# Performance work log

Hardware: AMD Instinct MI355X
Metric: run time of the kernel (lower is better)

The kernel has to match this reference:

```python
import jax, jax.numpy as jnp
import numpy as np

N = 100000      # num_nodes
E = 3200000     # num_edges (avg degree 32)
DIN, DH, DOUT = 128, 128, 64
S, L = 3, 3     # num_scales, num_layers
EPS = 1e-5


def setup_inputs() -> dict:
    key = jax.random.key(0)
    ks = jax.random.split(key, 12)
    sc = 0.05
    x = jax.random.normal(ks[0], (N, DIN), jnp.float32)
    edge_index = jax.random.randint(ks[1], (2, E), 0, N, jnp.int32)
    return {
        'x': x,
        'edge_index': edge_index,
        'W0': jax.random.normal(ks[2], (S, DIN, DH), jnp.float32) * sc,
        'b0': jnp.zeros((S, DH), jnp.float32),
        'W1': jax.random.normal(ks[3], (S, DH, DH), jnp.float32) * sc,
        'b1': jnp.zeros((S, DH), jnp.float32),
        'W2': jax.random.normal(ks[4], (S, DH, DOUT), jnp.float32) * sc,
        'b2': jnp.zeros((S, DOUT), jnp.float32),
        'gamma': jnp.ones((S * L, DH), jnp.float32),   # layer_norms (only first L-1 per scale used)
        'beta': jnp.zeros((S * L, DH), jnp.float32),
        'Wf': jax.random.normal(ks[5], (S * DOUT, DOUT), jnp.float32) * sc,
        'bf': jnp.zeros((DOUT,), jnp.float32),
    }


def _layer_norm(h, g, b):
    mu = jnp.mean(h, axis=-1, keepdims=True)
    var = jnp.mean(jnp.square(h - mu), axis=-1, keepdims=True)
    return (h - mu) * jax.lax.rsqrt(var + EPS) * g + b


def _gcn(h, W, b, src, dst, dis):
    # GCNConv: D^{-1/2}(A+I)D^{-1/2} h W + b  (self-loops handled separately)
    hw = h @ W
    msg = hw[src] * (dis[src] * dis[dst])[:, None]          # gather + edge-scale
    agg = jax.ops.segment_sum(msg, dst, num_segments=N)     # scatter-add
    agg = agg + hw * (dis * dis)[:, None]                   # self-loop term
    return agg + b


def reference(x, edge_index, W0, b0, W1, b1, W2, b2, gamma, beta, Wf, bf):
    src, dst = edge_index[0], edge_index[1]
    # degree on A + I (unit edge weights + self loop)
    deg = jax.ops.segment_sum(jnp.ones((E,), x.dtype), dst, num_segments=N) + 1.0
    dis = jax.lax.rsqrt(deg)

    scale_outputs = []
    for s in range(S):
        h = _gcn(x, W0[s], b0[s], src, dst, dis)
        h = _layer_norm(jax.nn.relu(h), gamma[s * L + 0], beta[s * L + 0])  # dropout=identity (eval)
        h = _gcn(h, W1[s], b1[s], src, dst, dis)
        h = _layer_norm(jax.nn.relu(h), gamma[s * L + 1], beta[s * L + 1])
        h = _gcn(h, W2[s], b2[s], src, dst, dis)
        scale_outputs.append(h)

    fused = jnp.concatenate(scale_outputs, axis=-1)  # [N, S*DOUT]
    return fused @ Wf + bf
```

## Files before the change

### kernel.cpp

```cpp
#include <hip/hip_runtime.h>

#define DIN 128
#define DH 128
#define DOUTC 64
#define NS 3
#define NL 3
#define EPSV 1e-5f

typedef __attribute__((ext_vector_type(8))) short bf16x8;
typedef __attribute__((ext_vector_type(4))) float f32x4;

static __device__ inline float bf2f(unsigned short h) {
    unsigned int u = ((unsigned int)h) << 16;
    return __builtin_bit_cast(float, u);
}
static __device__ inline unsigned short f2bf(float f) {
    unsigned int u = __builtin_bit_cast(unsigned int, f);
    u += 0x7fffu + ((u >> 16) & 1u);
    return (unsigned short)(u >> 16);
}
static __device__ inline float lo16(unsigned int u) {
    return __builtin_bit_cast(float, u << 16);
}
static __device__ inline float hi16(unsigned int u) {
    return __builtin_bit_cast(float, u & 0xffff0000u);
}

__global__ __launch_bounds__(256) void k_count_r(const int* __restrict__ dst,
                                                 int* __restrict__ counts, int e, int n) {
    int rg = blockIdx.x & 7;
    int lo = rg * (n >> 3);
    int hi = (rg == 7) ? n : lo + (n >> 3);
    int nb = gridDim.x >> 3, bi = blockIdx.x >> 3;
    int e4 = e >> 2;
    const int4* dst4 = (const int4*)dst;
    for (int i = bi * 256 + threadIdx.x; i < e4; i += nb * 256) {
        int4 d = dst4[i];
        if (d.x >= lo && d.x < hi) atomicAdd(&counts[d.x], 1);
        if (d.y >= lo && d.y < hi) atomicAdd(&counts[d.y], 1);
        if (d.z >= lo && d.z < hi) atomicAdd(&counts[d.z], 1);
        if (d.w >= lo && d.w < hi) atomicAdd(&counts[d.w], 1);
    }
    if (bi == 0 && (int)threadIdx.x < (e & 3)) {
        int d = dst[e4 * 4 + threadIdx.x];
        if (d >= lo && d < hi) atomicAdd(&counts[d], 1);
    }
}

__global__ void k_dis(const int* __restrict__ counts, float* __restrict__ dis, int n) {
    int i = blockIdx.x * blockDim.x + threadIdx.x;
    if (i < n) dis[i] = rsqrtf((float)counts[i] + 1.0f);
}

__global__ void k_scanA(const int* __restrict__ counts, int* __restrict__ row_start,
                        int* __restrict__ bsums, int n) {
    __shared__ int s[512];
    int t = threadIdx.x;
    int i = blockIdx.x * 512 + t;
    int v = (i < n) ? counts[i] : 0;
    s[t] = v;
    __syncthreads();
    for (int off = 1; off < 512; off <<= 1) {
        int x = s[t];
        if (t >= off) x += s[t - off];
        __syncthreads();
        s[t] = x;
        __syncthreads();
    }
    if (i < n) row_start[i] = s[t] - v;
    if (t == 511) bsums[blockIdx.x] = s[511];
}

__global__ void k_scanB(int* __restrict__ bsums, int nb) {
    __shared__ int s[256];
    int t = threadIdx.x;
    int v = (t < nb) ? bsums[t] : 0;
    s[t] = v;
    __syncthreads();
    for (int off = 1; off < 256; off <<= 1) {
        int x = s[t];
        if (t >= off) x += s[t - off];
        __syncthreads();
        s[t] = x;
        __syncthreads();
    }
    if (t < nb) bsums[t] = s[t] - v;
}

__global__ void k_scanC(int* __restrict__ row_start, const int* __restrict__ bsums, int n) {
    int i = blockIdx.x * blockDim.x + threadIdx.x;
    if (i < n) row_start[i] += bsums[i >> 9];
}

__global__ __launch_bounds__(256) void k_fill_r(const int* __restrict__ src,
                                                const int* __restrict__ dst,
                                                int* __restrict__ cursor,
                                                int* __restrict__ col, int e, int n) {
    int rg = blockIdx.x & 7;
    int lo = rg * (n >> 3);
    int hi = (rg == 7) ? n : lo + (n >> 3);
    int nb = gridDim.x >> 3, bi = blockIdx.x >> 3;
    int e4 = e >> 2;
    const int4* dst4 = (const int4*)dst;
    const int4* src4 = (const int4*)src;
    for (int i = bi * 256 + threadIdx.x; i < e4; i += nb * 256) {
        int4 d = dst4[i];
        int4 s = src4[i];
        if (d.x >= lo && d.x < hi) col[atomicAdd(&cursor[d.x], 1)] = s.x;
        if (d.y >= lo && d.y < hi) col[atomicAdd(&cursor[d.y], 1)] = s.y;
        if (d.z >= lo && d.z < hi) col[atomicAdd(&cursor[d.z], 1)] = s.z;
        if (d.w >= lo && d.w < hi) col[atomicAdd(&cursor[d.w], 1)] = s.w;
    }
    if (bi == 0 && (int)threadIdx.x < (e & 3)) {
        int d = dst[e4 * 4 + threadIdx.x];
        int s = src[e4 * 4 + threadIdx.x];
        if (d >= lo && d < hi) col[atomicAdd(&cursor[d], 1)] = s;
    }
}

__global__ void k_prep_w(const float* __restrict__ W0, const float* __restrict__ W1,
                         const float* __restrict__ W2, const float* __restrict__ Wf,
                         const float* __restrict__ b2, const float* __restrict__ bf,
                         unsigned short* __restrict__ Wt0hi, unsigned short* __restrict__ Wt0lo,
                         unsigned short* __restrict__ Wt1hi, unsigned short* __restrict__ Wt1lo,
                         unsigned short* __restrict__ Mhi, unsigned short* __restrict__ Mlo,
                         float* __restrict__ bcomb) {
    int idx = blockIdx.x * blockDim.x + threadIdx.x;
    if (idx < NS * DH * DH) {
        int s = idx / (DH * DH);
        int rem = idx % (DH * DH);
        int o = rem / DH, i = rem % DH;
        {
            float v = W0[(size_t)s * DH * DH + (size_t)i * DH + o];
            unsigned short h = f2bf(v);
            Wt0hi[idx] = h;
            Wt0lo[idx] = f2bf(v - bf2f(h));
        }
        {
            float v = W1[(size_t)s * DH * DH + (size_t)i * DH + o];
            unsigned short h = f2bf(v);
            Wt1hi[idx] = h;
            Wt1lo[idx] = f2bf(v - bf2f(h));
        }
    }
    if (idx < DOUTC * NS * DH) {
        int o = idx / (NS * DH);
        int k = idx % (NS * DH);
        int s = k / DH, i = k % DH;
        float acc = 0.f;
        for (int c = 0; c < DOUTC; ++c)
            acc += W2[((size_t)s * DH + i) * DOUTC + c] * Wf[((size_t)s * DOUTC + c) * DOUTC + o];
        unsigned short h = f2bf(acc);
        Mhi[idx] = h;
        Mlo[idx] = f2bf(acc - bf2f(h));
    }
    if (idx < DOUTC) {
        float acc = bf[idx];
        for (int s = 0; s < NS; ++s)
            for (int c = 0; c < DOUTC; ++c)
                acc += b2[s * DOUTC + c] * Wf[((size_t)s * DOUTC + c) * DOUTC + idx];
        bcomb[idx] = acc;
    }
}

__global__ void k_cvt(const float2* __restrict__ x, unsigned int* __restrict__ xb,
                      const float* __restrict__ dis, int m) {
    int i = blockIdx.x * blockDim.x + threadIdx.x;
    int stride = gridDim.x * blockDim.x;
    for (; i < m; i += stride) {
        float d = dis[i >> 6];
        float2 v = x[i];
        xb[i] = ((unsigned int)f2bf(v.y * d) << 16) | f2bf(v.x * d);
    }
}

__global__ __launch_bounds__(256) void k_agg128(
        const unsigned int* __restrict__ in, unsigned int* __restrict__ out,
        const float* __restrict__ dis, const int* __restrict__ rowstart,
        const int* __restrict__ counts, const int* __restrict__ col, int n) {
    int wid = (blockIdx.x * blockDim.x + threadIdx.x) >> 6;
    int lane = threadIdx.x & 63;
    int nw = (gridDim.x * blockDim.x) >> 6;
    for (int v = wid; v < n; v += nw) {
        float dv = dis[v];
        const int* colp = col + rowstart[v];
        int cnt = counts[v];
        unsigned int us = in[(size_t)v * 64 + lane];
        float a0 = lo16(us), a1 = hi16(us);
        int i = 0;
        for (; i + 4 <= cnt; i += 4) {
            int s0 = colp[i], s1 = colp[i + 1], s2 = colp[i + 2], s3 = colp[i + 3];
            unsigned int u0 = in[(size_t)s0 * 64 + lane];
            unsigned int u1 = in[(size_t)s1 * 64 + lane];
            unsigned int u2 = in[(size_t)s2 * 64 + lane];
            unsigned int u3 = in[(size_t)s3 * 64 + lane];
            a0 += lo16(u0); a1 += hi16(u0);
            a0 += lo16(u1); a1 += hi16(u1);
            a0 += lo16(u2); a1 += hi16(u2);
            a0 += lo16(u3); a1 += hi16(u3);
        }
        for (; i < cnt; ++i) {
            unsigned int u0 = in[(size_t)colp[i] * 64 + lane];
            a0 += lo16(u0); a1 += hi16(u0);
        }
        out[(size_t)v * 64 + lane] = ((unsigned int)f2bf(dv * a1) << 16) | f2bf(dv * a0);
    }
}

__global__ __launch_bounds__(256) void k_agg384(
        const unsigned int* __restrict__ in, unsigned int* __restrict__ out,
        const float* __restrict__ dis, const int* __restrict__ rowstart,
        const int* __restrict__ counts, const int* __restrict__ col, int n) {
    int wid = (blockIdx.x * blockDim.x + threadIdx.x) >> 6;
    int lane = threadIdx.x & 63;
    int nw = (gridDim.x * blockDim.x) >> 6;
    for (int v = wid; v < n; v += nw) {
        float dv = dis[v];
        const int* colp = col + rowstart[v];
        int cnt = counts[v];
        const unsigned int* ps = in + (size_t)v * 192;
        unsigned int us0 = ps[lane], us1 = ps[lane + 64], us2 = ps[lane + 128];
        float a0 = lo16(us0), a1 = hi16(us0);
        float a2 = lo16(us1), a3 = hi16(us1);
        float a4 = lo16(us2), a5 = hi16(us2);
        int i = 0;
        for (; i + 4 <= cnt; i += 4) {
            int s0 = colp[i], s1 = colp[i + 1], s2 = colp[i + 2], s3 = colp[i + 3];
            const unsigned int* p0 = in + (size_t)s0 * 192;
            const unsigned int* p1 = in + (size_t)s1 * 192;
            const unsigned int* p2 = in + (size_t)s2 * 192;
            const unsigned int* p3 = in + (size_t)s3 * 192;
            unsigned int u00 = p0[lane], u01 = p0[lane + 64], u02 = p0[lane + 128];
            unsigned int u10 = p1[lane], u11 = p1[lane + 64], u12 = p1[lane + 128];
            unsigned int u20 = p2[lane], u21 = p2[lane + 64], u22 = p2[lane + 128];
            unsigned int u30 = p3[lane], u31 = p3[lane + 64], u32 = p3[lane + 128];
            a0 += lo16(u00); a1 += hi16(u00);
            a2 += lo16(u01); a3 += hi16(u01);
            a4 += lo16(u02); a5 += hi16(u02);
            a0 += lo16(u10); a1 += hi16(u10);
            a2 += lo16(u11); a3 += hi16(u11);
            a4 += lo16(u12); a5 += hi16(u12);
            a0 += lo16(u20); a1 += hi16(u20);
            a2 += lo16(u21); a3 += hi16(u21);
            a4 += lo16(u22); a5 += hi16(u22);
            a0 += lo16(u30); a1 += hi16(u30);
            a2 += lo16(u31); a3 += hi16(u31);
            a4 += lo16(u32); a5 += hi16(u32);
        }
        for (; i < cnt; ++i) {
            const unsigned int* p0 = in + (size_t)colp[i] * 192;
            unsigned int u00 = p0[lane], u01 = p0[lane + 64], u02 = p0[lane + 128];
            a0 += lo16(u00); a1 += hi16(u00);
            a2 += lo16(u01); a3 += hi16(u01);
            a4 += lo16(u02); a5 += hi16(u02);
        }
        unsigned int* po = out + (size_t)v * 192;
        po[lane]       = ((unsigned int)f2bf(dv * a1) << 16) | f2bf(dv * a0);
        po[lane + 64]  = ((unsigned int)f2bf(dv * a3) << 16) | f2bf(dv * a2);
        po[lane + 128] = ((unsigned int)f2bf(dv * a5) << 16) | f2bf(dv * a4);
    }
}

__global__ __launch_bounds__(256) void k_agg64(
        const unsigned int* __restrict__ in, float* __restrict__ out,
        const float* __restrict__ bcomb, const float* __restrict__ dis,
        const int* __restrict__ rowstart, const int* __restrict__ counts,
        const int* __restrict__ col, int n) {
    int wid = (blockIdx.x * blockDim.x + threadIdx.x) >> 6;
    int lane = threadIdx.x & 63;
    int half = lane >> 5, c = lane & 31;
    int nw = (gridDim.x * blockDim.x) >> 6;
    float bc0 = bcomb[c * 2], bc1 = bcomb[c * 2 + 1];
    for (int w = wid; w * 2 < n; w += nw) {
        int v = w * 2 + half;
        if (v >= n) continue;
        float dv = dis[v];
        const int* colp = col + rowstart[v];
        int cnt = counts[v];
        unsigned int us = in[(size_t)v * 32 + c];
        float a0 = lo16(us), a1 = hi16(us);
        int i = 0;
        for (; i + 4 <= cnt; i += 4) {
            int s0 = colp[i], s1 = colp[i + 1], s2 = colp[i + 2], s3 = colp[i + 3];
            unsigned int u0 = in[(size_t)s0 * 32 + c];
            unsigned int u1 = in[(size_t)s1 * 32 + c];
            unsigned int u2 = in[(size_t)s2 * 32 + c];
            unsigned int u3 = in[(size_t)s3 * 32 + c];
            a0 += lo16(u0); a1 += hi16(u0);
            a0 += lo16(u1); a1 += hi16(u1);
            a0 += lo16(u2); a1 += hi16(u2);
            a0 += lo16(u3); a1 += hi16(u3);
        }
        for (; i < cnt; ++i) {
            unsigned int u0 = in[(size_t)colp[i] * 32 + c];
            a0 += lo16(u0); a1 += hi16(u0);
        }
        float2 o = make_float2(dv * a0 + bc0, dv * a1 + bc1);
        *(float2*)&out[(size_t)v * 64 + c * 2] = o;
    }
}

__global__ __launch_bounds__(256) void k_gemm0(
        const unsigned short* __restrict__ A, const unsigned short* __restrict__ Whi,
        const unsigned short* __restrict__ Wlo, const float* __restrict__ bias,
        const float* __restrict__ gamma, const float* __restrict__ beta,
        const float* __restrict__ dis, unsigned short* __restrict__ out, int n) {
    int wave = threadIdx.x >> 6, lane = threadIdx.x & 63;
    int g = blockIdx.x * 4 + wave;
    if (g * 16 >= n) return;
    int r16 = lane & 15, g4 = lane >> 4;
    int row = g * 16 + r16;
    if (row >= n) row = n - 1;

    bf16x8 a[4];
    #pragma unroll
    for (int ks = 0; ks < 4; ++ks)
        a[ks] = *(const bf16x8*)&A[(size_t)row * DH + ks * 32 + g4 * 8];

    for (int s = 0; s < NS; ++s) {
        const unsigned short* whi = Whi + (size_t)s * DH * DH;
        const unsigned short* wlo = Wlo + (size_t)s * DH * DH;
        f32x4 acc[8];
        #pragma unroll
        for (int t = 0; t < 8; ++t) acc[t] = (f32x4){0.f, 0.f, 0.f, 0.f};
        #pragma unroll
        for (int ks = 0; ks < 4; ++ks) {
            #pragma unroll
            for (int t = 0; t < 8; ++t) {
                size_t wofs = (size_t)(t * 16 + r16) * DH + ks * 32 + g4 * 8;
                bf16x8 bh = *(const bf16x8*)&whi[wofs];
                bf16x8 bl = *(const bf16x8*)&wlo[wofs];
                acc[t] = __builtin_amdgcn_mfma_f32_16x16x32_bf16(a[ks], bh, acc[t], 0, 0, 0);
                acc[t] = __builtin_amdgcn_mfma_f32_16x16x32_bf16(a[ks], bl, acc[t], 0, 0, 0);
            }
        }
        float bia[8], gam[8], bet[8];
        #pragma unroll
        for (int t = 0; t < 8; ++t) {
            bia[t] = bias[s * DH + t * 16 + r16];
            gam[t] = gamma[(size_t)(s * NL + 0) * DH + t * 16 + r16];
            bet[t] = beta[(size_t)(s * NL + 0) * DH + t * 16 + r16];
        }
        #pragma unroll
        for (int r = 0; r < 4; ++r) {
            float y[8];
            float sm = 0.f, q = 0.f;
            #pragma unroll
            for (int t = 0; t < 8; ++t) {
                y[t] = fmaxf(acc[t][r] + bia[t], 0.f);
                sm += y[t];
                q += y[t] * y[t];
            }
            #pragma unroll
            for (int off = 8; off; off >>= 1) {
                sm += __shfl_xor(sm, off);
                q += __shfl_xor(q, off);
            }
            float mu = sm * (1.f / 128.f);
            float var = q * (1.f / 128.f) - mu * mu;
            float rstd = rsqrtf(var + EPSV);
            int node = g * 16 + g4 * 4 + r;
            if (node < n) {
                float dnode = dis[node];
                #pragma unroll
                for (int t = 0; t < 8; ++t) {
                    float o = ((y[t] - mu) * rstd * gam[t] + bet[t]) * dnode;
                    out[(size_t)node * (NS * DH) + s * DH + t * 16 + r16] = f2bf(o);
                }
            }
        }
    }
}

__global__ __launch_bounds__(256) void k_gemm1q(
        const unsigned short* __restrict__ G, const unsigned short* __restrict__ Whi,
        const unsigned short* __restrict__ Wlo, const unsigned short* __restrict__ Mhi,
        const unsigned short* __restrict__ Mlo, const float* __restrict__ bias,
        const float* __restrict__ gamma, const float* __restrict__ beta,
        const float* __restrict__ dis, unsigned short* __restrict__ q, int n) {
    __shared__ __align__(16) unsigned short sH[4][16][392];
    int wave = threadIdx.x >> 6, lane = threadIdx.x & 63;
    int g = blockIdx.x * 4 + wave;
    if (g * 16 >= n) return;
    int r16 = lane & 15, g4 = lane >> 4;
    int row = g * 16 + r16;
    if (row >= n) row = n - 1;

    for (int s = 0; s < NS; ++s) {
        bf16x8 a[4];
        #pragma unroll
        for (int ks = 0; ks < 4; ++ks)
            a[ks] = *(const bf16x8*)&G[(size_t)row * (NS * DH) + s * DH + ks * 32 + g4 * 8];
        const unsigned short* whi = Whi + (size_t)s * DH * DH;
        const unsigned short* wlo = Wlo + (size_t)s * DH * DH;
        f32x4 acc[8];
        #pragma unroll
        for (int t = 0; t < 8; ++t) acc[t] = (f32x4){0.f, 0.f, 0.f, 0.f};
        #pragma unroll
        for (int ks = 0; ks < 4; ++ks) {
            #pragma unroll
            for (int t = 0; t < 8; ++t) {
                size_t wofs = (size_t)(t * 16 + r16) * DH + ks * 32 + g4 * 8;
                bf16x8 bh = *(const bf16x8*)&whi[wofs];
                bf16x8 bl = *(const bf16x8*)&wlo[wofs];
                acc[t] = __builtin_amdgcn_mfma_f32_16x16x32_bf16(a[ks], bh, acc[t], 0, 0, 0);
                acc[t] = __builtin_amdgcn_mfma_f32_16x16x32_bf16(a[ks], bl, acc[t], 0, 0, 0);
            }
        }
        float bia[8], gam[8], bet[8];
        #pragma unroll
        for (int t = 0; t < 8; ++t) {
            bia[t] = bias[s * DH + t * 16 + r16];
            gam[t] = gamma[(size_t)(s * NL + 1) * DH + t * 16 + r16];
            bet[t] = beta[(size_t)(s * NL + 1) * DH + t * 16 + r16];
        }
        #pragma unroll
        for (int r = 0; r < 4; ++r) {
            float y[8];
            float sm = 0.f, qq = 0.f;
            #pragma unroll
            for (int t = 0; t < 8; ++t) {
                y[t] = fmaxf(acc[t][r] + bia[t], 0.f);
                sm += y[t];
                qq += y[t] * y[t];
            }
            #pragma unroll
            for (int off = 8; off; off >>= 1) {
                sm += __shfl_xor(sm, off);
                qq += __shfl_xor(qq, off);
            }
            float mu = sm * (1.f / 128.f);
            float var = qq * (1.f / 128.f) - mu * mu;
            float rstd = rsqrtf(var + EPSV);
            #pragma unroll
            for (int t = 0; t < 8; ++t) {
                float o = (y[t] - mu) * rstd * gam[t] + bet[t];
                sH[wave][g4 * 4 + r][s * DH + t * 16 + r16] = f2bf(o);
            }
        }
    }
    __syncthreads();
    f32x4 qa[4];
    #pragma unroll
    for (int t = 0; t < 4; ++t) qa[t] = (f32x4){0.f, 0.f, 0.f, 0.f};
    #pragma unroll
    for (int ks = 0; ks < 12; ++ks) {
        bf16x8 av = *(const bf16x8*)&sH[wave][r16][ks * 32 + g4 * 8];
        #pragma unroll
        for (int t = 0; t < 4; ++t) {
            size_t wofs = (size_t)(t * 16 + r16) * (NS * DH) + ks * 32 + g4 * 8;
            bf16x8 bh = *(const bf16x8*)&Mhi[wofs];
            bf16x8 bl = *(const bf16x8*)&Mlo[wofs];
            qa[t] = __builtin_amdgcn_mfma_f32_16x16x32_bf16(av, bh, qa[t], 0, 0, 0);
            qa[t] = __builtin_amdgcn_mfma_f32_16x16x32_bf16(av, bl, qa[t], 0, 0, 0);
        }
    }
    #pragma unroll
    for (int r = 0; r < 4; ++r) {
        int node = g * 16 + g4 * 4 + r;
        if (node < n) {
            float dnode = dis[node];
            #pragma unroll
            for (int t = 0; t < 4; ++t)
                q[(size_t)node * DOUTC + t * 16 + r16] = f2bf(qa[t][r] * dnode);
        }
    }
}

extern "C" void kernel_launch(void* const* d_in, const int* in_sizes, int n_in,
                              void* d_out, int out_size, void* d_ws, size_t ws_size,
                              hipStream_t stream) {
    const float* x    = (const float*)d_in[0];
    const int*   ei   = (const int*)d_in[1];
    const float* W0   = (const float*)d_in[2];
    const float* b0   = (const float*)d_in[3];
    const float* W1   = (const float*)d_in[4];
    const float* b1   = (const float*)d_in[5];
    const float* W2   = (const float*)d_in[6];
    const float* b2   = (const float*)d_in[7];
    const float* gamma= (const float*)d_in[8];
    const float* beta = (const float*)d_in[9];
    const float* Wf   = (const float*)d_in[10];
    const float* bf   = (const float*)d_in[11];
    float* out = (float*)d_out;

    const int n = in_sizes[0] / DIN;
    const int e = in_sizes[1] / 2;
    const int* src = ei;
    const int* dst = ei + e;

    char* ws = (char*)d_ws;
    auto alloc = [&](size_t bytes) {
        char* p = ws;
        ws += (bytes + 255) & ~(size_t)255;
        return p;
    };
    int*   counts   = (int*)alloc((size_t)n * 4);
    int*   cursor   = (int*)alloc((size_t)n * 4);
    int*   rowstart = (int*)alloc((size_t)n * 4);
    int*   bsums    = (int*)alloc(4096);
    float* dis      = (float*)alloc((size_t)n * 4);
    int*   col      = (int*)alloc((size_t)e * 4);
    unsigned short* Wt0hi = (unsigned short*)alloc((size_t)NS * DH * DH * 2);
    unsigned short* Wt0lo = (unsigned short*)alloc((size_t)NS * DH * DH * 2);
    unsigned short* Wt1hi = (unsigned short*)alloc((size_t)NS * DH * DH * 2);
    unsigned short* Wt1lo = (unsigned short*)alloc((size_t)NS * DH * DH * 2);
    unsigned short* Mhi   = (unsigned short*)alloc((size_t)DOUTC * NS * DH * 2);
    unsigned short* Mlo   = (unsigned short*)alloc((size_t)DOUTC * NS * DH * 2);
    float* bcomb    = (float*)alloc(DOUTC * 4);
    unsigned short* xb    = (unsigned short*)alloc((size_t)n * DIN * 2);
    unsigned short* z0    = (unsigned short*)alloc((size_t)n * DH * 2);
    unsigned short* h1cat = (unsigned short*)alloc((size_t)n * NS * DH * 2);
    unsigned short* g1cat = (unsigned short*)alloc((size_t)n * NS * DH * 2);
    unsigned short* q     = (unsigned short*)alloc((size_t)n * DOUTC * 2);

    hipMemsetAsync(counts, 0, (size_t)n * 4, stream);

    k_count_r<<<2048, 256, 0, stream>>>(dst, counts, e, n);
    k_dis<<<(n + 255) / 256, 256, 0, stream>>>(counts, dis, n);

    int nb = (n + 511) / 512;
    k_scanA<<<nb, 512, 0, stream>>>(counts, rowstart, bsums, n);
    k_scanB<<<1, 256, 0, stream>>>(bsums, nb);
    k_scanC<<<(n + 255) / 256, 256, 0, stream>>>(rowstart, bsums, n);
    hipMemcpyAsync(cursor, rowstart, (size_t)n * 4, hipMemcpyDeviceToDevice, stream);
    k_fill_r<<<2048, 256, 0, stream>>>(src, dst, cursor, col, e, n);

    k_prep_w<<<(NS * DH * DH + 255) / 256, 256, 0, stream>>>(
        W0, W1, W2, Wf, b2, bf, Wt0hi, Wt0lo, Wt1hi, Wt1lo, Mhi, Mlo, bcomb);
    k_cvt<<<2048, 256, 0, stream>>>((const float2*)x, (unsigned int*)xb, dis, n * DIN / 2);

    k_agg128<<<2048, 256, 0, stream>>>((const unsigned int*)xb, (unsigned int*)z0,
                                       dis, rowstart, counts, col, n);
    const int GG = (n / 16 + 3) / 4;
    k_gemm0<<<GG, 256, 0, stream>>>(z0, Wt0hi, Wt0lo, b0, gamma, beta, dis, h1cat, n);
    k_agg384<<<2048, 256, 0, stream>>>((const unsigned int*)h1cat, (unsigned int*)g1cat,
                                       dis, rowstart, counts, col, n);
    k_gemm1q<<<GG, 256, 0, stream>>>(g1cat, Wt1hi, Wt1lo, Mhi, Mlo,
                                     b1, gamma, beta, dis, q, n);
    k_agg64<<<2048, 256, 0, stream>>>((const unsigned int*)q, out, bcomb,
                                      dis, rowstart, counts, col, n);
}
```

Measured before the change: 1.403 ms.

## Quantize gathered node features to int8 with per-row scales in all aggregations

New measurement: 1.242 ms. 1.13x faster.

```diff
diff --git a/kernel.cpp b/kernel.cpp
--- a/kernel.cpp
+++ b/kernel.cpp
@@ -24,6 +24,17 @@
 }
 static __device__ inline float hi16(unsigned int u) {
     return __builtin_bit_cast(float, u & 0xffff0000u);
+}
+static __device__ inline unsigned int pkbf(float lo, float hi) {
+    return ((unsigned int)f2bf(hi) << 16) | f2bf(lo);
+}
+static __device__ inline float sext8(unsigned int u, int k) {
+    return (float)((int)(u << (24 - 8 * k)) >> 24);
+}
+static __device__ inline unsigned int pk8(float a, float b, float c, float d, float qs) {
+    int q0 = (int)rintf(a * qs), q1 = (int)rintf(b * qs);
+    int q2 = (int)rintf(c * qs), q3 = (int)rintf(d * qs);
+    return (q0 & 255) | ((q1 & 255) << 8) | ((q2 & 255) << 16) | ((q3 & 255) << 24);
 }
 
 __global__ __launch_bounds__(256) void k_count_r(const int* __restrict__ dst,
@@ -163,140 +174,223 @@
     }
 }
 
-__global__ void k_cvt(const float2* __restrict__ x, unsigned int* __restrict__ xb,
-                      const float* __restrict__ dis, int m) {
-    int i = blockIdx.x * blockDim.x + threadIdx.x;
-    int stride = gridDim.x * blockDim.x;
-    for (; i < m; i += stride) {
-        float d = dis[i >> 6];
-        float2 v = x[i];
-        xb[i] = ((unsigned int)f2bf(v.y * d) << 16) | f2bf(v.x * d);
-    }
-}
-
-__global__ __launch_bounds__(256) void k_agg128(
-        const unsigned int* __restrict__ in, unsigned int* __restrict__ out,
-        const float* __restrict__ dis, const int* __restrict__ rowstart,
-        const int* __restrict__ counts, const int* __restrict__ col, int n) {
-    int wid = (blockIdx.x * blockDim.x + threadIdx.x) >> 6;
+__global__ __launch_bounds__(256) void k_cvtq(const float2* __restrict__ x,
+                                              unsigned int* __restrict__ xq,
+                                              float* __restrict__ xs,
+                                              const float* __restrict__ dis, int n) {
+    int wid = ((blockIdx.x * blockDim.x + threadIdx.x) >> 6);
     int lane = threadIdx.x & 63;
-    int nw = (gridDim.x * blockDim.x) >> 6;
-    for (int v = wid; v < n; v += nw) {
-        float dv = dis[v];
-        const int* colp = col + rowstart[v];
-        int cnt = counts[v];
-        unsigned int us = in[(size_t)v * 64 + lane];
-        float a0 = lo16(us), a1 = hi16(us);
-        int i = 0;
-        for (; i + 4 <= cnt; i += 4) {
-            int s0 = colp[i], s1 = colp[i + 1], s2 = colp[i + 2], s3 = colp[i + 3];
-            unsigned int u0 = in[(size_t)s0 * 64 + lane];
-            unsigned int u1 = in[(size_t)s1 * 64 + lane];
-            unsigned int u2 = in[(size_t)s2 * 64 + lane];
-            unsigned int u3 = in[(size_t)s3 * 64 + lane];
-            a0 += lo16(u0); a1 += hi16(u0);
-            a0 += lo16(u1); a1 += hi16(u1);
-            a0 += lo16(u2); a1 += hi16(u2);
-            a0 += lo16(u3); a1 += hi16(u3);
-        }
-        for (; i < cnt; ++i) {
-            unsigned int u0 = in[(size_t)colp[i] * 64 + lane];
-            a0 += lo16(u0); a1 += hi16(u0);
-        }
-        out[(size_t)v * 64 + lane] = ((unsigned int)f2bf(dv * a1) << 16) | f2bf(dv * a0);
-    }
-}
-
-__global__ __launch_bounds__(256) void k_agg384(
-        const unsigned int* __restrict__ in, unsigned int* __restrict__ out,
-        const float* __restrict__ dis, const int* __restrict__ rowstart,
-        const int* __restrict__ counts, const int* __restrict__ col, int n) {
-    int wid = (blockIdx.x * blockDim.x + threadIdx.x) >> 6;
+    if (wid >= n) return;
+    float2 v = x[(size_t)wid * 64 + lane];
+    float m = fmaxf(fabsf(v.x), fabsf(v.y));
+    #pragma unroll
+    for (int off = 32; off; off >>= 1) m = fmaxf(m, __shfl_xor(m, off));
+    float qs = m > 0.f ? 127.f / m : 0.f;
+    int q0 = (int)rintf(v.x * qs), q1 = (int)rintf(v.y * qs);
+    ((unsigned short*)xq)[(size_t)wid * 64 + lane] =
+        (unsigned short)((q0 & 255) | ((q1 & 255) << 8));
+    if (lane == 0) xs[wid] = dis[wid] * m * (1.f / 127.f);
+}
+
+__global__ __launch_bounds__(256) void k_quant384(const unsigned int* __restrict__ h,
+                                                  unsigned int* __restrict__ hq,
+                                                  float* __restrict__ hs, int n) {
+    int wid = ((blockIdx.x * blockDim.x + threadIdx.x) >> 6);
     int lane = threadIdx.x & 63;
-    int nw = (gridDim.x * blockDim.x) >> 6;
-    for (int v = wid; v < n; v += nw) {
-        float dv = dis[v];
-        const int* colp = col + rowstart[v];
-        int cnt = counts[v];
-        const unsigned int* ps = in + (size_t)v * 192;
-        unsigned int us0 = ps[lane], us1 = ps[lane + 64], us2 = ps[lane + 128];
-        float a0 = lo16(us0), a1 = hi16(us0);
-        float a2 = lo16(us1), a3 = hi16(us1);
-        float a4 = lo16(us2), a5 = hi16(us2);
-        int i = 0;
-        for (; i + 4 <= cnt; i += 4) {
-            int s0 = colp[i], s1 = colp[i + 1], s2 = colp[i + 2], s3 = colp[i + 3];
-            const unsigned int* p0 = in + (size_t)s0 * 192;
-            const unsigned int* p1 = in + (size_t)s1 * 192;
-            const unsigned int* p2 = in + (size_t)s2 * 192;
-            const unsigned int* p3 = in + (size_t)s3 * 192;
-            unsigned int u00 = p0[lane], u01 = p0[lane + 64], u02 = p0[lane + 128];
-            unsigned int u10 = p1[lane], u11 = p1[lane + 64], u12 = p1[lane + 128];
-            unsigned int u20 = p2[lane], u21 = p2[lane + 64], u22 = p2[lane + 128];
-            unsigned int u30 = p3[lane], u31 = p3[lane + 64], u32 = p3[lane + 128];
-            a0 += lo16(u00); a1 += hi16(u00);
-            a2 += lo16(u01); a3 += hi16(u01);
-            a4 += lo16(u02); a5 += hi16(u02);
-            a0 += lo16(u10); a1 += hi16(u10);
-            a2 += lo16(u11); a3 += hi16(u11);
-            a4 += lo16(u12); a5 += hi16(u12);
-            a0 += lo16(u20); a1 += hi16(u20);
-            a2 += lo16(u21); a3 += hi16(u21);
-            a4 += lo16(u22); a5 += hi16(u22);
-            a0 += lo16(u30); a1 += hi16(u30);
-            a2 += lo16(u31); a3 += hi16(u31);
-            a4 += lo16(u32); a5 += hi16(u32);
-        }
-        for (; i < cnt; ++i) {
-            const unsigned int* p0 = in + (size_t)colp[i] * 192;
-            unsigned int u00 = p0[lane], u01 = p0[lane + 64], u02 = p0[lane + 128];
-            a0 += lo16(u00); a1 += hi16(u00);
-            a2 += lo16(u01); a3 += hi16(u01);
-            a4 += lo16(u02); a5 += hi16(u02);
-        }
-        unsigned int* po = out + (size_t)v * 192;
-        po[lane]       = ((unsigned int)f2bf(dv * a1) << 16) | f2bf(dv * a0);
-        po[lane + 64]  = ((unsigned int)f2bf(dv * a3) << 16) | f2bf(dv * a2);
-        po[lane + 128] = ((unsigned int)f2bf(dv * a5) << 16) | f2bf(dv * a4);
-    }
-}
-
-__global__ __launch_bounds__(256) void k_agg64(
-        const unsigned int* __restrict__ in, float* __restrict__ out,
-        const float* __restrict__ bcomb, const float* __restrict__ dis,
+    int half = lane >> 5, c = lane & 31;
+    int v = wid * 2 + half;
+    if (v >= n) return;
+    const uint2* p = (const uint2*)(h + (size_t)v * 192);
+    uint2 w0 = p[c], w1 = p[c + 32], w2 = p[c + 64];
+    float f[12] = {lo16(w0.x), hi16(w0.x), lo16(w0.y), hi16(w0.y),
+                   lo16(w1.x), hi16(w1.x), lo16(w1.y), hi16(w1.y),
+                   lo16(w2.x), hi16(w2.x), lo16(w2.y), hi16(w2.y)};
+    float m = 0.f;
+    #pragma unroll
+    for (int k = 0; k < 12; ++k) m = fmaxf(m, fabsf(f[k]));
+    #pragma unroll
+    for (int off = 16; off; off >>= 1) m = fmaxf(m, __shfl_xor(m, off));
+    float qs = m > 0.f ? 127.f / m : 0.f;
+    unsigned int* po = hq + (size_t)v * 96;
+    po[c]      = pk8(f[0], f[1], f[2], f[3], qs);
+    po[c + 32] = pk8(f[4], f[5], f[6], f[7], qs);
+    po[c + 64] = pk8(f[8], f[9], f[10], f[11], qs);
+    if (c == 0) hs[v] = m * (1.f / 127.f);
+}
+
+__global__ __launch_bounds__(256) void k_quant64(const unsigned int* __restrict__ qb,
+                                                 unsigned int* __restrict__ qq,
+                                                 float* __restrict__ qs2, int n) {
+    int wid = ((blockIdx.x * blockDim.x + threadIdx.x) >> 6);
+    int lane = threadIdx.x & 63;
+    int g = lane >> 4, c = lane & 15;
+    int v = wid * 4 + g;
+    if (v >= n) return;
+    uint2 w = ((const uint2*)(qb + (size_t)v * 32))[c];
+    float f0 = lo16(w.x), f1 = hi16(w.x), f2 = lo16(w.y), f3 = hi16(w.y);
+    float m = fmaxf(fmaxf(fabsf(f0), fabsf(f1)), fmaxf(fabsf(f2), fabsf(f3)));
+    #pragma unroll
+    for (int off = 8; off; off >>= 1) m = fmaxf(m, __shfl_xor(m, off));
+    float qs = m > 0.f ? 127.f / m : 0.f;
+    qq[(size_t)v * 16 + c] = pk8(f0, f1, f2, f3, qs);
+    if (c == 0) qs2[v] = m * (1.f / 127.f);
+}
+
+__global__ __launch_bounds__(256) void k_agg128q(
+        const unsigned int* __restrict__ xq, const float* __restrict__ xs,
+        unsigned int* __restrict__ z0, const float* __restrict__ dis,
         const int* __restrict__ rowstart, const int* __restrict__ counts,
         const int* __restrict__ col, int n) {
     int wid = (blockIdx.x * blockDim.x + threadIdx.x) >> 6;
     int lane = threadIdx.x & 63;
     int half = lane >> 5, c = lane & 31;
     int nw = (gridDim.x * blockDim.x) >> 6;
-    float bc0 = bcomb[c * 2], bc1 = bcomb[c * 2 + 1];
-    for (int w = wid; w * 2 < n; w += nw) {
+    int ntask = (n + 1) >> 1;
+    for (int w = wid; w < ntask; w += nw) {
         int v = w * 2 + half;
-        if (v >= n) continue;
-        float dv = dis[v];
-        const int* colp = col + rowstart[v];
-        int cnt = counts[v];
-        unsigned int us = in[(size_t)v * 32 + c];
-        float a0 = lo16(us), a1 = hi16(us);
+        int vc = v < n ? v : n - 1;
+        float dv = dis[vc];
+        const int* colp = col + rowstart[vc];
+        int cnt = v < n ? counts[vc] : 0;
+        unsigned int us = xq[(size_t)vc * 32 + c];
+        float sv = xs[vc];
+        float a0 = sv * sext8(us, 0), a1 = sv * sext8(us, 1);
+        float a2 = sv * sext8(us, 2), a3 = sv * sext8(us, 3);
+        int i = 0;
+        for (; i + 8 <= cnt; i += 8) {
+            #pragma unroll
+            for (int k = 0; k < 8; ++k) {
+                int s0 = colp[i + k];
+                float sc = xs[s0];
+                unsigned int u = xq[(size_t)s0 * 32 + c];
+                a0 += sc * sext8(u, 0); a1 += sc * sext8(u, 1);
+                a2 += sc * sext8(u, 2); a3 += sc * sext8(u, 3);
+            }
+        }
+        for (; i < cnt; ++i) {
+            int s0 = colp[i];
+            float sc = xs[s0];
+            unsigned int u = xq[(size_t)s0 * 32 + c];
+            a0 += sc * sext8(u, 0); a1 += sc * sext8(u, 1);
+            a2 += sc * sext8(u, 2); a3 += sc * sext8(u, 3);
+        }
+        if (v < n) {
+            uint2 o = {pkbf(dv * a0, dv * a1), pkbf(dv * a2, dv * a3)};
+            *(uint2*)&z0[(size_t)v * 64 + 2 * c] = o;
+        }
+    }
+}
+
+__global__ __launch_bounds__(256) void k_agg384q(
+        const unsigned int* __restrict__ hq, const float* __restrict__ hs,
+        unsigned int* __restrict__ g1, const float* __restrict__ dis,
+        const int* __restrict__ rowstart, const int* __restrict__ counts,
+        const int* __restrict__ col, int n) {
+    int wid = (blockIdx.x * blockDim.x + threadIdx.x) >> 6;
+    int lane = threadIdx.x & 63;
+    int half = lane >> 5, c = lane & 31;
+    int nw = (gridDim.x * blockDim.x) >> 6;
+    int ntask = (n + 1) >> 1;
+    for (int w = wid; w < ntask; w += nw) {
+        int v = w * 2 + half;
+        int vc = v < n ? v : n - 1;
+        float dv = dis[vc];
+        const int* colp = col + rowstart[vc];
+        int cnt = v < n ? counts[vc] : 0;
+        const unsigned int* rp = hq + (size_t)vc * 96;
+        unsigned int u0 = rp[c], u1 = rp[c + 32], u2 = rp[c + 64];
+        float sv = hs[vc];
+        float a[12];
+        #pragma unroll
+        for (int k = 0; k < 4; ++k) {
+            a[k]     = sv * sext8(u0, k);
+            a[4 + k] = sv * sext8(u1, k);
+            a[8 + k] = sv * sext8(u2, k);
+        }
         int i = 0;
         for (; i + 4 <= cnt; i += 4) {
-            int s0 = colp[i], s1 = colp[i + 1], s2 = colp[i + 2], s3 = colp[i + 3];
-            unsigned int u0 = in[(size_t)s0 * 32 + c];
-            unsigned int u1 = in[(size_t)s1 * 32 + c];
-            unsigned int u2 = in[(size_t)s2 * 32 + c];
-            unsigned int u3 = in[(size_t)s3 * 32 + c];
-            a0 += lo16(u0); a1 += hi16(u0);
-            a0 += lo16(u1); a1 += hi16(u1);
-            a0 += lo16(u2); a1 += hi16(u2);
-            a0 += lo16(u3); a1 += hi16(u3);
+            #pragma unroll
+            for (int k4 = 0; k4 < 4; ++k4) {
+                int s0 = colp[i + k4];
+                float sc = hs[s0];
+                const unsigned int* p0 = hq + (size_t)s0 * 96;
+                unsigned int w0 = p0[c], w1 = p0[c + 32], w2 = p0[c + 64];
+                #pragma unroll
+                for (int k = 0; k < 4; ++k) {
+                    a[k]     += sc * sext8(w0, k);
+                    a[4 + k] += sc * sext8(w1, k);
+                    a[8 + k] += sc * sext8(w2, k);
+                }
+            }
         }
         for (; i < cnt; ++i) {
-            unsigned int u0 = in[(size_t)colp[i] * 32 + c];
-            a0 += lo16(u0); a1 += hi16(u0);
-        }
-        float2 o = make_float2(dv * a0 + bc0, dv * a1 + bc1);
-        *(float2*)&out[(size_t)v * 64 + c * 2] = o;
+            int s0 = colp[i];
+            float sc = hs[s0];
+            const unsigned int* p0 = hq + (size_t)s0 * 96;
+            unsigned int w0 = p0[c], w1 = p0[c + 32], w2 = p0[c + 64];
+            #pragma unroll
+            for (int k = 0; k < 4; ++k) {
+                a[k]     += sc * sext8(w0, k);
+                a[4 + k] += sc * sext8(w1, k);
+                a[8 + k] += sc * sext8(w2, k);
+            }
+        }
+        if (v < n) {
+            unsigned int* po = g1 + (size_t)v * 192;
+            uint2 o0 = {pkbf(dv * a[0], dv * a[1]), pkbf(dv * a[2], dv * a[3])};
+            *(uint2*)&po[2 * c] = o0;
+            uint2 o1 = {pkbf(dv * a[4], dv * a[5]), pkbf(dv * a[6], dv * a[7])};
+            *(uint2*)&po[2 * c + 64] = o1;
+            uint2 o2 = {pkbf(dv * a[8], dv * a[9]), pkbf(dv * a[10], dv * a[11])};
+            *(uint2*)&po[2 * c + 128] = o2;
+        }
+    }
+}
+
+__global__ __launch_bounds__(256) void k_agg64q(
+        const unsigned int* __restrict__ qq, const float* __restrict__ qs2,
+        float* __restrict__ out, const float* __restrict__ bcomb,
+        const float* __restrict__ dis, const int* __restrict__ rowstart,
+        const int* __restrict__ counts, const int* __restrict__ col, int n) {
+    int wid = (blockIdx.x * blockDim.x + threadIdx.x) >> 6;
+    int lane = threadIdx.x & 63;
+    int g = lane >> 4, c = lane & 15;
+    int nw = (gridDim.x * blockDim.x) >> 6;
+    int ntask = (n + 3) >> 2;
+    float4 bc = ((const float4*)bcomb)[c];
+    for (int w = wid; w < ntask; w += nw) {
+        int v = w * 4 + g;
+        int vc = v < n ? v : n - 1;
+        float dv = dis[vc];
+        const int* colp = col + rowstart[vc];
+        int cnt = v < n ? counts[vc] : 0;
+        unsigned int us = qq[(size_t)vc * 16 + c];
+        float sv = qs2[vc];
+        float a0 = sv * sext8(us, 0), a1 = sv * sext8(us, 1);
+        float a2 = sv * sext8(us, 2), a3 = sv * sext8(us, 3);
+        int i = 0;
+        for (; i + 8 <= cnt; i += 8) {
+            #pragma unroll
+            for (int k = 0; k < 8; ++k) {
+                int s0 = colp[i + k];
+                float sc = qs2[s0];
+                unsigned int u = qq[(size_t)s0 * 16 + c];
+                a0 += sc * sext8(u, 0); a1 += sc * sext8(u, 1);
+                a2 += sc * sext8(u, 2); a3 += sc * sext8(u, 3);
+            }
+        }
+        for (; i < cnt; ++i) {
+            int s0 = colp[i];
+            float sc = qs2[s0];
+            unsigned int u = qq[(size_t)s0 * 16 + c];
+            a0 += sc * sext8(u, 0); a1 += sc * sext8(u, 1);
+            a2 += sc * sext8(u, 2); a3 += sc * sext8(u, 3);
+        }
+        if (v < n) {
+            float4 o = make_float4(dv * a0 + bc.x, dv * a1 + bc.y,
+                                   dv * a2 + bc.z, dv * a3 + bc.w);
+            *(float4*)&out[(size_t)v * 64 + 4 * c] = o;
+        }
     }
 }
 
@@ -508,11 +602,16 @@
     unsigned short* Mhi   = (unsigned short*)alloc((size_t)DOUTC * NS * DH * 2);
     unsigned short* Mlo   = (unsigned short*)alloc((size_t)DOUTC * NS * DH * 2);
     float* bcomb    = (float*)alloc(DOUTC * 4);
-    unsigned short* xb    = (unsigned short*)alloc((size_t)n * DIN * 2);
+    unsigned int* xq  = (unsigned int*)alloc((size_t)n * 32 * 4);
+    float* xs         = (float*)alloc((size_t)n * 4);
     unsigned short* z0    = (unsigned short*)alloc((size_t)n * DH * 2);
     unsigned short* h1cat = (unsigned short*)alloc((size_t)n * NS * DH * 2);
+    unsigned int* h1q = (unsigned int*)alloc((size_t)n * 96 * 4);
+    float* hs         = (float*)alloc((size_t)n * 4);
     unsigned short* g1cat = (unsigned short*)alloc((size_t)n * NS * DH * 2);
     unsigned short* q     = (unsigned short*)alloc((size_t)n * DOUTC * 2);
+    unsigned int* qq  = (unsigned int*)alloc((size_t)n * 16 * 4);
+    float* qs2        = (float*)alloc((size_t)n * 4);
 
     hipMemsetAsync(counts, 0, (size_t)n * 4, stream);
 
@@ -528,16 +627,18 @@
 
     k_prep_w<<<(NS * DH * DH + 255) / 256, 256, 0, stream>>>(
         W0, W1, W2, Wf, b2, bf, Wt0hi, Wt0lo, Wt1hi, Wt1lo, Mhi, Mlo, bcomb);
-    k_cvt<<<2048, 256, 0, stream>>>((const float2*)x, (unsigned int*)xb, dis, n * DIN / 2);
-
-    k_agg128<<<2048, 256, 0, stream>>>((const unsigned int*)xb, (unsigned int*)z0,
-                                       dis, rowstart, counts, col, n);
+    k_cvtq<<<(n + 3) / 4, 256, 0, stream>>>((const float2*)x, xq, xs, dis, n);
+
+    k_agg128q<<<2048, 256, 0, stream>>>(xq, xs, (unsigned int*)z0,
+                                        dis, rowstart, counts, col, n);
     const int GG = (n / 16 + 3) / 4;
     k_gemm0<<<GG, 256, 0, stream>>>(z0, Wt0hi, Wt0lo, b0, gamma, beta, dis, h1cat, n);
-    k_agg384<<<2048, 256, 0, stream>>>((const unsigned int*)h1cat, (unsigned int*)g1cat,
-                                       dis, rowstart, counts, col, n);
+    k_quant384<<<(n + 7) / 8, 256, 0, stream>>>((const unsigned int*)h1cat, h1q, hs, n);
+    k_agg384q<<<2048, 256, 0, stream>>>(h1q, hs, (unsigned int*)g1cat,
+                                        dis, rowstart, counts, col, n);
     k_gemm1q<<<GG, 256, 0, stream>>>(g1cat, Wt1hi, Wt1lo, Mhi, Mlo,
                                      b1, gamma, beta, dis, q, n);
-    k_agg64<<<2048, 256, 0, stream>>>((const unsigned int*)q, out, bcomb,
-                                      dis, rowstart, counts, col, n);
-}
+    k_quant64<<<(n + 15) / 16, 256, 0, stream>>>((const unsigned int*)q, qq, qs2, n);
+    k_agg64q<<<2048, 256, 0, stream>>>(qq, qs2, out, bcomb,
+                                       dis, rowstart, counts, col, n);
+}
```
